# Kernel optimization log

Measured on AMD Instinct MI355X. Metric: run time of the kernel, lower is better.

## Reference

```python
import jax, jax.numpy as jnp
import numpy as np

B, S, H, R, G, L, A = 1024, 512, 2048, 64, 16, 4, 256
ADAPT_SCALE = 0.1


def setup_inputs() -> dict:
    key = jax.random.key(0)
    ks = jax.random.split(key, 12)
    w = lambda k, shp: (jax.random.normal(k, shp, dtype=jnp.float32) * 0.02)
    return {
        "s": jax.random.normal(ks[0], (B, S), dtype=jnp.float32),
        "W_in": w(ks[1], (S, H)),
        "b_in": jnp.zeros((H,), jnp.float32),
        "W_main": w(ks[2], (L, H, H)),
        "b_main": jnp.zeros((L, H), jnp.float32),
        "Wa": w(ks[3], (L, G, H, R)),   # down-projection per layer/group
        "ba": jnp.zeros((L, G, R), jnp.float32),
        "Wb": w(ks[4], (L, G, R, H)),   # up-projection per layer/group
        "bb": jnp.zeros((L, G, H), jnp.float32),
        "W_out": w(ks[5], (H, A)),
        "b_out": jnp.zeros((A,), jnp.float32),
    }


def reference(s, W_in, b_in, W_main, b_main, Wa, ba, Wb, bb, W_out, b_out):
    # g=None path: expand state across groups, then input layer (group-invariant)
    x = s @ W_in + b_in                              # [B, H]
    x = jnp.broadcast_to(x[:, None, :], (B, G, H))   # [B, G, H]
    for i in range(L):
        h = jnp.einsum("bgh,hk->bgk", x, W_main[i]) + b_main[i]          # shared main GEMM
        z = jnp.einsum("bgh,ghr->bgr", x, Wa[i]) + ba[i]                  # grouped low-rank down
        z = jnp.einsum("bgr,grh->bgh", z, Wb[i]) + bb[i]                  # grouped low-rank up
        h = h + ADAPT_SCALE * z
        x = jax.nn.elu(h)                            # dropout in eval mode = identity
    logits = jnp.einsum("bgh,ha->bga", x, W_out) + b_out  # Categorical(logits=...)
    return logits
```

## Files before the change

kernel.cpp:

```cpp
#include <hip/hip_runtime.h>
#include <cstdint>
#include <cmath>

typedef _Float16 f16;
typedef _Float16 f16x8 __attribute__((ext_vector_type(8)));
typedef float f32x4 __attribute__((ext_vector_type(4)));

#define DEVI static __device__ __forceinline__

constexpr int B_ = 1024, S_ = 512, H_ = 2048, R_ = 64, G_ = 16, L_ = 4, A_ = 256;
constexpr float ADAPT = 0.1f;

DEVI void gl_lds16(const void* g, void* l) {
  __builtin_amdgcn_global_load_lds((const __attribute__((address_space(1))) void*)g,
                                   (__attribute__((address_space(3))) void*)l,
                                   16, 0, 0);
}

template <int N> DEVI void wvc() {
  if constexpr (N == 0)       asm volatile("s_waitcnt vmcnt(0)");
  else if constexpr (N == 2)  asm volatile("s_waitcnt vmcnt(2)");
  else if constexpr (N == 3)  asm volatile("s_waitcnt vmcnt(3)");
  else if constexpr (N == 4)  asm volatile("s_waitcnt vmcnt(4)");
  else if constexpr (N == 6)  asm volatile("s_waitcnt vmcnt(6)");
  else if constexpr (N == 8)  asm volatile("s_waitcnt vmcnt(8)");
  else if constexpr (N == 9)  asm volatile("s_waitcnt vmcnt(9)");
  else if constexpr (N == 12) asm volatile("s_waitcnt vmcnt(12)");
  else static_assert(N == 0, "unsupported vmcnt literal");
}

__global__ void cvt_f16_kernel(const float* __restrict__ src, f16* __restrict__ dst, int n) {
  int i = blockIdx.x * blockDim.x + threadIdx.x;
  if (i < n) dst[i] = (f16)src[i];
}

__global__ void transpose_cvt_kernel(const float* __restrict__ src, f16* __restrict__ dst,
                                     int rows, int cols, float scale) {
  src += (size_t)blockIdx.z * rows * cols;
  dst += (size_t)blockIdx.z * rows * cols;
  __shared__ float tile[32][33];
  const int tx = threadIdx.x, ty = threadIdx.y;
  const int r0 = blockIdx.y * 32, c0 = blockIdx.x * 32;
  #pragma unroll
  for (int i = ty; i < 32; i += 8)
    tile[i][tx] = src[(size_t)(r0 + i) * cols + (c0 + tx)];
  __syncthreads();
  #pragma unroll
  for (int i = ty; i < 32; i += 8)
    dst[(size_t)(c0 + i) * rows + (r0 + tx)] = (f16)(tile[tx][i] * scale);
}


#define MQ(QM, QN, AF, BF)                                                   \
  _Pragma("unroll") for (int i = 0; i < 4; ++i)                              \
  _Pragma("unroll") for (int j = 0; j < 2; ++j)                              \
  _Pragma("unroll") for (int k = 0; k < 2; ++k)                              \
    acc[QM][QN][i][j] = __builtin_amdgcn_mfma_f32_16x16x32_f16(              \
        AF[i][k], BF[j][k], acc[QM][QN][i][j], 0, 0, 0)

#define STGM(BASE, OFF, DST) do {                                            \
    gl_lds16(BASE + OFF, &lds[DST]);                                         \
    gl_lds16(BASE + OFF + 32768, &lds[DST + 1024]);                          \
    OFF += 128; DST ^= 65536; } while (0)
#define STGC(BASE, OFF, DST) do {                                            \
    gl_lds16(BASE + OFF, &lds[DST]);                                         \
    gl_lds16(BASE + OFF + 1024, &lds[DST + 1024]);                           \
    DST ^= 65536; } while (0)
#define NOSTG ((void)0)
#define WV6 asm volatile("s_waitcnt vmcnt(6)")
#define WV0 asm volatile("s_waitcnt vmcnt(0)")
#define NOW ((void)0)
#define BAR() __builtin_amdgcn_s_barrier()
#define PRI1 __builtin_amdgcn_s_setprio(1)
#define PRI0 __builtin_amdgcn_s_setprio(0)

#define TILE_V0(PC, S1, S2, S3, S4, BW) do {                                 \
    f16x8 a0[4][2], a1[4][2], b0[2][2], b1v[2][2];                           \
    _Pragma("unroll") for (int i = 0; i < 4; ++i) {                          \
      a0[i][0] = *(const f16x8*)&lds[(PC) + cab + i * 2048 + lof0];          \
      a0[i][1] = *(const f16x8*)&lds[(PC) + cab + i * 2048 + lof1]; }        \
    _Pragma("unroll") for (int j = 0; j < 2; ++j) {                          \
      b0[j][0] = *(const f16x8*)&lds[(PC) + cbb + j * 2048 + lof0];          \
      b0[j][1] = *(const f16x8*)&lds[(PC) + cbb + j * 2048 + lof1]; }        \
    S1; BAR();                                                               \
    PRI1; MQ(0, 0, a0, b0); PRI0; BAR();                                     \
    _Pragma("unroll") for (int j = 0; j < 2; ++j) {                          \
      b1v[j][0] = *(const f16x8*)&lds[(PC) + cbb + 16384 + j * 2048 + lof0]; \
      b1v[j][1] = *(const f16x8*)&lds[(PC) + cbb + 16384 + j * 2048 + lof1]; } \
    S2; BAR();                                                               \
    PRI1; MQ(0, 1, a0, b1v); PRI0; BAR();                                    \
    _Pragma("unroll") for (int i = 0; i < 4; ++i) {                          \
      a1[i][0] = *(const f16x8*)&lds[(PC) + cab + 16384 + i * 2048 + lof0];  \
      a1[i][1] = *(const f16x8*)&lds[(PC) + cab + 16384 + i * 2048 + lof1]; } \
    S3; BAR();                                                               \
    PRI1; MQ(1, 1, a1, b1v); PRI0; BAR();                                    \
    S4; BAR();                                                               \
    PRI1; MQ(1, 0, a1, b0); PRI0;                                            \
    BW; BAR();                                                               \
  } while (0)

__global__ __launch_bounds__(512, 2)
void gemm8_main_kernel(const f16* __restrict__ Aacts,
                      const f16* __restrict__ Wm,
                      const f16* __restrict__ Z1,
                      const f16* __restrict__ Wb2,
                      const float* __restrict__ b1,
                      const float* __restrict__ b2,
                      f16* __restrict__ Out) {
  __shared__ __align__(16) char lds[131072];
  const int tid = threadIdx.x, lane = tid & 63, wid = tid >> 6;
  const int swz = (blockIdx.x & 7) * 64 + (blockIdx.x >> 3);
  const int bm0 = (swz & 63) * 256, bn0 = (swz >> 6) * 256;
  const int g = bm0 >> 10;
  const char* GA = (const char*)Aacts;
  const char* GB = (const char*)Wm;
  const char* GZ = (const char*)Z1;
  const char* GW2 = (const char*)(Wb2 + (size_t)g * H_ * R_);
  const float* b2g = b2 + (size_t)g * H_;

  const int srow8 = lane >> 3;
  const int scolb = ((lane & 7) ^ srow8) * 16;
  const int fr = lane & 15, fq = lane >> 4;
  const uint32_t lof0 = fr * 128 + ((fq * 16) ^ ((fr & 7) << 4));
  const uint32_t lof1 = lof0 ^ 64;

  const uint32_t rA0 = bm0 + wid * 16 + srow8;
  const uint32_t rB0 = bn0 + wid * 16 + srow8;
  uint32_t oA0 = rA0 * 4096 + scolb;
  uint32_t oA1 = oA0 + 128 * 4096;
  uint32_t oB0 = rB0 * 4096 + scolb;
  uint32_t oB1 = oB0 + 128 * 4096;
  uint32_t dA0 = wid * 2048;
  uint32_t dA1 = 16384 + wid * 2048;
  uint32_t dB0 = 32768 + wid * 2048;
  uint32_t dB1 = 49152 + wid * 2048;
  const uint32_t cab = (wid >> 2) * 8192;
  const uint32_t cbb = 32768 + (wid & 3) * 4096;

  f32x4 acc[2][2][4][2] = {};

  STGM(GA, oA0, dA0);
  STGM(GB, oB0, dB0);
  STGM(GA, oA1, dA1);
  STGM(GB, oB1, dB1);
  STGM(GA, oA0, dA0);
  STGM(GB, oB0, dB0);
  STGM(GA, oA1, dA1);
  WV6;
  BAR();

  uint32_t oA0c = rA0 * 128 + scolb;
  uint32_t oA1c = oA0c + 128 * 128;
  uint32_t oB0c = rB0 * 128 + scolb;
  uint32_t oB1c = oB0c + 128 * 128;

  #pragma unroll 1
  for (int it = 0; it < 15; ++it) {
    TILE_V0(0,
            STGM(GB, oB1, dB1), STGM(GA, oA0, dA0),
            STGM(GB, oB0, dB0), STGM(GA, oA1, dA1), WV6);
    TILE_V0(65536,
            STGM(GB, oB1, dB1), STGM(GA, oA0, dA0),
            STGM(GB, oB0, dB0), STGM(GA, oA1, dA1), WV6);
  }
  TILE_V0(0,
          STGM(GB, oB1, dB1), STGC(GZ, oA0c, dA0),
          STGC(GW2, oB0c, dB0), STGC(GZ, oA1c, dA1), WV6);
  TILE_V0(65536,
          STGC(GW2, oB1c, dB1), NOSTG, NOSTG, NOSTG, WV0);
  TILE_V0(0, NOSTG, NOSTG, NOSTG, NOSTG, NOW);

  #pragma unroll
  for (int Qn = 0; Qn < 2; ++Qn) {
    #pragma unroll
    for (int j = 0; j < 2; ++j) {
      const int col = bn0 + Qn * 128 + (wid & 3) * 32 + j * 16 + fr;
      const float bb1 = b1[col];
      const float bb2 = ADAPT * b2g[col];
      #pragma unroll
      for (int Qm = 0; Qm < 2; ++Qm) {
        #pragma unroll
        for (int i = 0; i < 4; ++i) {
          #pragma unroll
          for (int r = 0; r < 4; ++r) {
            const int row = bm0 + Qm * 128 + (wid >> 2) * 64 + i * 16 + fq * 4 + r;
            float v = acc[Qm][Qn][i][j][r] + bb1 + bb2;
            v = v > 0.f ? v : expm1f(v);
            Out[(size_t)row * H_ + col] = (f16)v;
          }
        }
      }
    }
  }
}

enum { EPI_Z1 = 0, EPI_OUT = 1, EPI_L0 = 2 };

template <int BM, int BN, int WM, int WN, int EPI>
__global__ __launch_bounds__((BM / WM) * (BN / WN) * 64)
void gemm_db_kernel(const f16* __restrict__ A, long long lda, long long Az,
                    const f16* __restrict__ Bw, long long ldb, long long Bz,
                    long long Bg, int NT,
                    const float* __restrict__ bias1, long long b1z,
                    const float* __restrict__ bias2, long long b2z,
                    const f16* __restrict__ addmat,
                    void* __restrict__ outp, long long out_z, long long ldo,
                    int rows_per_group) {
  constexpr int NW = (BM / WM) * (BN / WN);
  constexpr int FM = WM / 16, FN = WN / 16;
  constexpr int RA = BM / (NW * 16), RB = BN / (NW * 16);
  constexpr int LPT = RA + RB;
  const int tid = threadIdx.x, lane = tid & 63, wid = tid >> 6;
  const int bm0 = blockIdx.x * BM, bn0 = blockIdx.y * BN;
  const int z = blockIdx.z;
  const int gidx = (rows_per_group > 0) ? (bm0 / rows_per_group) : 0;

  __shared__ __align__(16) f16 As[4][BM * 32];
  __shared__ __align__(16) f16 Bs[4][BN * 32];

  const int wm0 = (wid / (BN / WN)) * WM;
  const int wn0 = (wid % (BN / WN)) * WN;
  const int srow = wid * 16 + (lane >> 2);
  const int scol = (lane & 3) * 8;
  const int fr = lane & 15, fq = lane >> 4;

  const f16* pa = A + (long long)z * Az + (long long)(bm0 + srow) * lda + scol;
  const f16* pb = Bw + (long long)z * Bz + (long long)gidx * Bg +
                  (long long)(bn0 + srow) * ldb + scol;
  const long long stA = (long long)(NW * 16) * lda;
  const long long stB = (long long)(NW * 16) * ldb;

  f32x4 acc[FM][FN] = {};

  auto stage = [&](int t) {
    const f16* qa = pa + t * 32;
    const f16* qb = pb + t * 32;
    const int b = t & 3;
    #pragma unroll
    for (int r = 0; r < RA; ++r)
      gl_lds16(qa + r * stA, &As[b][(r * NW + wid) * 512]);
    #pragma unroll
    for (int r = 0; r < RB; ++r)
      gl_lds16(qb + r * stB, &Bs[b][(r * NW + wid) * 512]);
  };
  auto comp = [&](int t) {
    const int b = t & 3;
    f16x8 af[FM], bf[FN];
    #pragma unroll
    for (int i = 0; i < FM; ++i)
      af[i] = *(const f16x8*)&As[b][(wm0 + i * 16 + fr) * 32 + fq * 8];
    #pragma unroll
    for (int j = 0; j < FN; ++j)
      bf[j] = *(const f16x8*)&Bs[b][(wn0 + j * 16 + fr) * 32 + fq * 8];
    #pragma unroll
    for (int i = 0; i < FM; ++i)
      #pragma unroll
      for (int j = 0; j < FN; ++j)
        acc[i][j] = __builtin_amdgcn_mfma_f32_16x16x32_f16(af[i], bf[j], acc[i][j], 0, 0, 0);
  };

  if (NT <= 4) {
    for (int t = 0; t < NT; ++t) stage(t);
    wvc<0>();
    BAR();
    for (int t = 0; t < NT; ++t) comp(t);
  } else {
    stage(0); stage(1); stage(2); stage(3);
    int t = 0;
    #pragma unroll 1
    for (; t < NT - 4; ++t) {
      wvc<3 * LPT>();
      BAR();
      comp(t);
      BAR();
      stage(t + 4);
    }
    wvc<3 * LPT>(); BAR(); comp(t); BAR(); ++t;
    wvc<2 * LPT>(); BAR(); comp(t); BAR(); ++t;
    wvc<1 * LPT>(); BAR(); comp(t); BAR(); ++t;
    wvc<0>();       BAR(); comp(t);
  }

  const float* b1p = bias1 ? bias1 + (long long)z * b1z : nullptr;
  const float* b2p = bias2 ? bias2 + (long long)gidx * b2z : nullptr;
  #pragma unroll
  for (int i = 0; i < FM; ++i) {
    #pragma unroll
    for (int j = 0; j < FN; ++j) {
      const int col = bn0 + wn0 + j * 16 + fr;
      const float b1 = b1p ? b1p[col] : 0.f;
      const float b2v = b2p ? ADAPT * b2p[col] : 0.f;
      #pragma unroll
      for (int r = 0; r < 4; ++r) {
        const int row = bm0 + wm0 + i * 16 + fq * 4 + r;
        float v = acc[i][j][r] + b1 + b2v;
        if constexpr (EPI == EPI_L0) {
          v += (float)addmat[(long long)(row & (B_ - 1)) * H_ + col];
          v = v > 0.f ? v : expm1f(v);
          ((f16*)outp)[(long long)row * ldo + col] = (f16)v;
        } else if constexpr (EPI == EPI_Z1) {
          ((f16*)outp)[(long long)z * out_z + (long long)row * ldo + col] = (f16)v;
        } else {
          const int g = row >> 10, b = row & 1023;
          ((float*)outp)[((long long)b * G_ + g) * A_ + col] = v;
        }
      }
    }
  }
}

extern "C" void kernel_launch(void* const* d_in, const int* in_sizes, int n_in,
                              void* d_out, int out_size, void* d_ws, size_t ws_size,
                              hipStream_t stream) {
  const float* s      = (const float*)d_in[0];
  const float* W_in   = (const float*)d_in[1];
  const float* b_in   = (const float*)d_in[2];
  const float* W_main = (const float*)d_in[3];
  const float* b_main = (const float*)d_in[4];
  const float* Wa     = (const float*)d_in[5];
  const float* ba     = (const float*)d_in[6];
  const float* Wb     = (const float*)d_in[7];
  const float* bb     = (const float*)d_in[8];
  const float* W_out  = (const float*)d_in[9];
  const float* b_out  = (const float*)d_in[10];

  char* ws = (char*)d_ws;
  size_t off = 0;
  auto alloc = [&](size_t bytes) -> void* {
    void* p = ws + off;
    off += (bytes + 255) & ~(size_t)255;
    return p;
  };
  f16* sh   = (f16*)alloc((size_t)B_ * S_ * 2);
  f16* Wint = (f16*)alloc((size_t)H_ * S_ * 2);
  f16* Wmt  = (f16*)alloc((size_t)L_ * H_ * H_ * 2);
  f16* Wat  = (f16*)alloc((size_t)L_ * G_ * R_ * H_ * 2);
  f16* Wbt  = (f16*)alloc((size_t)L_ * G_ * H_ * R_ * 2);
  f16* Wot  = (f16*)alloc((size_t)A_ * H_ * 2);
  f16* xh0  = (f16*)alloc((size_t)G_ * B_ * H_ * 2);
  f16* xh1  = (f16*)alloc((size_t)G_ * B_ * H_ * 2);
  f16* z1h  = (f16*)alloc((size_t)G_ * B_ * R_ * 2);
  f16* x0h  = xh1;
  f16* y0h  = xh1 + (size_t)B_ * H_;

  cvt_f16_kernel<<<(B_ * S_ + 255) / 256, 256, 0, stream>>>(s, sh, B_ * S_);
  dim3 tb(32, 8);
  transpose_cvt_kernel<<<dim3(H_ / 32, S_ / 32, 1),   tb, 0, stream>>>(W_in,   Wint, S_, H_, 1.f);
  transpose_cvt_kernel<<<dim3(H_ / 32, H_ / 32, L_),  tb, 0, stream>>>(W_main, Wmt,  H_, H_, 1.f);
  transpose_cvt_kernel<<<dim3(R_ / 32, H_ / 32, L_ * G_), tb, 0, stream>>>(Wa, Wat, H_, R_, 1.f);
  transpose_cvt_kernel<<<dim3(H_ / 32, R_ / 32, L_ * G_), tb, 0, stream>>>(Wb, Wbt, R_, H_, ADAPT);
  transpose_cvt_kernel<<<dim3(A_ / 32, H_ / 32, 1),   tb, 0, stream>>>(W_out,  Wot,  H_, A_, 1.f);

  gemm_db_kernel<64, 128, 32, 64, EPI_Z1><<<dim3(B_ / 64, H_ / 128, 1), 256, 0, stream>>>(
      sh, S_, 0, Wint, S_, 0, 0, S_ / 32,
      b_in, 0, nullptr, 0, nullptr, x0h, 0, H_, 0);

  gemm_db_kernel<64, 128, 32, 64, EPI_Z1><<<dim3(B_ / 64, H_ / 128, 1), 256, 0, stream>>>(
      x0h, H_, 0, Wmt, H_, 0, 0, H_ / 32,
      b_main, 0, nullptr, 0, nullptr, y0h, 0, H_, 0);

  gemm_db_kernel<64, 64, 32, 32, EPI_Z1><<<dim3(B_ / 64, 1, G_), 256, 0, stream>>>(
      x0h, H_, 0, Wat, H_, (long long)R_ * H_, 0, H_ / 32,
      ba, R_, nullptr, 0, nullptr, z1h, (long long)B_ * R_, R_, 0);

  gemm_db_kernel<128, 128, 64, 64, EPI_L0><<<dim3(G_ * B_ / 128, H_ / 128, 1), 256, 0, stream>>>(
      z1h, R_, 0, Wbt, R_, 0, (long long)H_ * R_, R_ / 32,
      nullptr, 0, bb, H_, y0h, xh0, 0, H_, B_);

  f16* cur = xh0;
  f16* nxt = xh1;
  for (int l = 1; l < L_; ++l) {
    gemm_db_kernel<64, 64, 32, 32, EPI_Z1><<<dim3(B_ / 64, 1, G_), 256, 0, stream>>>(
        cur, H_, (long long)B_ * H_,
        Wat + (size_t)l * G_ * R_ * H_, H_, (long long)R_ * H_, 0, H_ / 32,
        ba + (size_t)l * G_ * R_, R_, nullptr, 0, nullptr,
        z1h, (long long)B_ * R_, R_, 0);
    gemm8_main_kernel<<<512, 512, 0, stream>>>(
        cur, Wmt + (size_t)l * H_ * H_, z1h, Wbt + (size_t)l * G_ * H_ * R_,
        b_main + (size_t)l * H_, bb + (size_t)l * G_ * H_, nxt);
    f16* t = cur; cur = nxt; nxt = t;
  }

  gemm_db_kernel<128, 128, 64, 64, EPI_OUT><<<dim3(G_ * B_ / 128, A_ / 128, 1), 256, 0, stream>>>(
      cur, H_, 0, Wot, H_, 0, 0, H_ / 32,
      b_out, 0, nullptr, 0, nullptr, d_out, 0, A_, 0);
}
```

Baseline: 760.5 us.

## Fuse weight prep kernels into one launch and restructure main GEMM prefetch schedule

Merges the f16 conversion and the five transpose-convert launches into one prep kernel that dispatches on block index, removing several kernel launches. The main GEMM tile loop goes from four barrier-separated MFMA phases to three, with the last two MFMA quadrants merged. Prefetch stages are now issued in pairs at two points per tile, and the pipeline depth drops from seven initial stages to six with vmcnt(4). This cuts barriers per tile but shortens the prefetch lookahead and adds divergent branching in the prep kernel.

```diff
diff --git a/kernel.cpp b/kernel.cpp
--- a/kernel.cpp
+++ b/kernel.cpp
@@ -19,6 +19,7 @@
 
 template <int N> DEVI void wvc() {
   if constexpr (N == 0)       asm volatile("s_waitcnt vmcnt(0)");
+  else if constexpr (N == 1)  asm volatile("s_waitcnt vmcnt(1)");
   else if constexpr (N == 2)  asm volatile("s_waitcnt vmcnt(2)");
   else if constexpr (N == 3)  asm volatile("s_waitcnt vmcnt(3)");
   else if constexpr (N == 4)  asm volatile("s_waitcnt vmcnt(4)");
@@ -29,18 +30,15 @@
   else static_assert(N == 0, "unsupported vmcnt literal");
 }
 
-__global__ void cvt_f16_kernel(const float* __restrict__ src, f16* __restrict__ dst, int n) {
-  int i = blockIdx.x * blockDim.x + threadIdx.x;
-  if (i < n) dst[i] = (f16)src[i];
-}
-
-__global__ void transpose_cvt_kernel(const float* __restrict__ src, f16* __restrict__ dst,
-                                     int rows, int cols, float scale) {
-  src += (size_t)blockIdx.z * rows * cols;
-  dst += (size_t)blockIdx.z * rows * cols;
-  __shared__ float tile[32][33];
+DEVI void tr_body(float (*tile)[33], const float* __restrict__ src, f16* __restrict__ dst,
+                  int rows, int cols, float scale, int bid) {
+  const int nx = cols / 32, ny = rows / 32;
+  const int z = bid / (nx * ny), rem = bid % (nx * ny);
+  const int cy = rem / nx, cx = rem % nx;
+  src += (size_t)z * rows * cols;
+  dst += (size_t)z * rows * cols;
   const int tx = threadIdx.x, ty = threadIdx.y;
-  const int r0 = blockIdx.y * 32, c0 = blockIdx.x * 32;
+  const int r0 = cy * 32, c0 = cx * 32;
   #pragma unroll
   for (int i = ty; i < 32; i += 8)
     tile[i][tx] = src[(size_t)(r0 + i) * cols + (c0 + tx)];
@@ -48,6 +46,31 @@
   #pragma unroll
   for (int i = ty; i < 32; i += 8)
     dst[(size_t)(c0 + i) * rows + (r0 + tx)] = (f16)(tile[tx][i] * scale);
+}
+
+__global__ void prep_kernel(const float* __restrict__ s, f16* __restrict__ sh,
+                            const float* __restrict__ W_in, f16* __restrict__ Wint,
+                            const float* __restrict__ W_main, f16* __restrict__ Wmt,
+                            const float* __restrict__ Wa, f16* __restrict__ Wat,
+                            const float* __restrict__ Wb, f16* __restrict__ Wbt,
+                            const float* __restrict__ W_out, f16* __restrict__ Wot) {
+  __shared__ float tile[32][33];
+  int bid = blockIdx.x;
+  if (bid < 2048) {
+    int i = bid * 256 + threadIdx.y * 32 + threadIdx.x;
+    sh[i] = (f16)s[i];
+    return;
+  }
+  bid -= 2048;
+  if (bid < 1024)  { tr_body(tile, W_in,   Wint, S_, H_, 1.f,   bid); return; }
+  bid -= 1024;
+  if (bid < 16384) { tr_body(tile, W_main, Wmt,  H_, H_, 1.f,   bid); return; }
+  bid -= 16384;
+  if (bid < 8192)  { tr_body(tile, Wa,     Wat,  H_, R_, 1.f,   bid); return; }
+  bid -= 8192;
+  if (bid < 8192)  { tr_body(tile, Wb,     Wbt,  R_, H_, ADAPT, bid); return; }
+  bid -= 8192;
+  tr_body(tile, W_out, Wot, H_, A_, 1.f, bid);
 }
 
 
@@ -67,14 +90,14 @@
     gl_lds16(BASE + OFF + 1024, &lds[DST + 1024]);                           \
     DST ^= 65536; } while (0)
 #define NOSTG ((void)0)
-#define WV6 asm volatile("s_waitcnt vmcnt(6)")
+#define WV4 asm volatile("s_waitcnt vmcnt(4)")
 #define WV0 asm volatile("s_waitcnt vmcnt(0)")
 #define NOW ((void)0)
 #define BAR() __builtin_amdgcn_s_barrier()
 #define PRI1 __builtin_amdgcn_s_setprio(1)
 #define PRI0 __builtin_amdgcn_s_setprio(0)
 
-#define TILE_V0(PC, S1, S2, S3, S4, BW) do {                                 \
+#define TILE3(PC, S1a, S1b, S2a, S2b, BW) do {                               \
     f16x8 a0[4][2], a1[4][2], b0[2][2], b1v[2][2];                           \
     _Pragma("unroll") for (int i = 0; i < 4; ++i) {                          \
       a0[i][0] = *(const f16x8*)&lds[(PC) + cab + i * 2048 + lof0];          \
@@ -82,20 +105,18 @@
     _Pragma("unroll") for (int j = 0; j < 2; ++j) {                          \
       b0[j][0] = *(const f16x8*)&lds[(PC) + cbb + j * 2048 + lof0];          \
       b0[j][1] = *(const f16x8*)&lds[(PC) + cbb + j * 2048 + lof1]; }        \
-    S1; BAR();                                                               \
+    S1a; S1b; BAR();                                                         \
     PRI1; MQ(0, 0, a0, b0); PRI0; BAR();                                     \
     _Pragma("unroll") for (int j = 0; j < 2; ++j) {                          \
       b1v[j][0] = *(const f16x8*)&lds[(PC) + cbb + 16384 + j * 2048 + lof0]; \
       b1v[j][1] = *(const f16x8*)&lds[(PC) + cbb + 16384 + j * 2048 + lof1]; } \
-    S2; BAR();                                                               \
+    S2a; S2b; BAR();                                                         \
     PRI1; MQ(0, 1, a0, b1v); PRI0; BAR();                                    \
     _Pragma("unroll") for (int i = 0; i < 4; ++i) {                          \
       a1[i][0] = *(const f16x8*)&lds[(PC) + cab + 16384 + i * 2048 + lof0];  \
       a1[i][1] = *(const f16x8*)&lds[(PC) + cab + 16384 + i * 2048 + lof1]; } \
-    S3; BAR();                                                               \
-    PRI1; MQ(1, 1, a1, b1v); PRI0; BAR();                                    \
-    S4; BAR();                                                               \
-    PRI1; MQ(1, 0, a1, b0); PRI0;                                            \
+    BAR();                                                                   \
+    PRI1; MQ(1, 1, a1, b1v); MQ(1, 0, a1, b0); PRI0;                         \
     BW; BAR();                                                               \
   } while (0)
 
@@ -145,8 +166,7 @@
   STGM(GB, oB1, dB1);
   STGM(GA, oA0, dA0);
   STGM(GB, oB0, dB0);
-  STGM(GA, oA1, dA1);
-  WV6;
+  WV4;
   BAR();
 
   uint32_t oA0c = rA0 * 128 + scolb;
@@ -156,19 +176,20 @@
 
   #pragma unroll 1
   for (int it = 0; it < 15; ++it) {
-    TILE_V0(0,
-            STGM(GB, oB1, dB1), STGM(GA, oA0, dA0),
-            STGM(GB, oB0, dB0), STGM(GA, oA1, dA1), WV6);
-    TILE_V0(65536,
-            STGM(GB, oB1, dB1), STGM(GA, oA0, dA0),
-            STGM(GB, oB0, dB0), STGM(GA, oA1, dA1), WV6);
-  }
-  TILE_V0(0,
-          STGM(GB, oB1, dB1), STGC(GZ, oA0c, dA0),
-          STGC(GW2, oB0c, dB0), STGC(GZ, oA1c, dA1), WV6);
-  TILE_V0(65536,
-          STGC(GW2, oB1c, dB1), NOSTG, NOSTG, NOSTG, WV0);
-  TILE_V0(0, NOSTG, NOSTG, NOSTG, NOSTG, NOW);
+    TILE3(0,
+          STGM(GB, oB1, dB1), STGM(GA, oA1, dA1),
+          STGM(GA, oA0, dA0), STGM(GB, oB0, dB0), WV4);
+    TILE3(65536,
+          STGM(GB, oB1, dB1), STGM(GA, oA1, dA1),
+          STGM(GA, oA0, dA0), STGM(GB, oB0, dB0), WV4);
+  }
+  TILE3(0,
+        STGM(GB, oB1, dB1), STGM(GA, oA1, dA1),
+        STGC(GZ, oA0c, dA0), STGC(GW2, oB0c, dB0), WV4);
+  TILE3(65536,
+        STGC(GW2, oB1c, dB1), STGC(GZ, oA1c, dA1),
+        NOSTG, NOSTG, WV0);
+  TILE3(0, NOSTG, NOSTG, NOSTG, NOSTG, NOW);
 
   #pragma unroll
   for (int Qn = 0; Qn < 2; ++Qn) {
@@ -343,13 +364,8 @@
   f16* x0h  = xh1;
   f16* y0h  = xh1 + (size_t)B_ * H_;
 
-  cvt_f16_kernel<<<(B_ * S_ + 255) / 256, 256, 0, stream>>>(s, sh, B_ * S_);
-  dim3 tb(32, 8);
-  transpose_cvt_kernel<<<dim3(H_ / 32, S_ / 32, 1),   tb, 0, stream>>>(W_in,   Wint, S_, H_, 1.f);
-  transpose_cvt_kernel<<<dim3(H_ / 32, H_ / 32, L_),  tb, 0, stream>>>(W_main, Wmt,  H_, H_, 1.f);
-  transpose_cvt_kernel<<<dim3(R_ / 32, H_ / 32, L_ * G_), tb, 0, stream>>>(Wa, Wat, H_, R_, 1.f);
-  transpose_cvt_kernel<<<dim3(H_ / 32, R_ / 32, L_ * G_), tb, 0, stream>>>(Wb, Wbt, R_, H_, ADAPT);
-  transpose_cvt_kernel<<<dim3(A_ / 32, H_ / 32, 1),   tb, 0, stream>>>(W_out,  Wot,  H_, A_, 1.f);
+  prep_kernel<<<36352, dim3(32, 8), 0, stream>>>(
+      s, sh, W_in, Wint, W_main, Wmt, Wa, Wat, Wb, Wbt, W_out, Wot);
 
   gemm_db_kernel<64, 128, 32, 64, EPI_Z1><<<dim3(B_ / 64, H_ / 128, 1), 256, 0, stream>>>(
       sh, S_, 0, Wint, S_, 0, 0, S_ / 32,
```

Result: faster. 743.4 us (-2.2%).
